# Optimization experiments

Measured on AMD Instinct MI355X. Metric: run time of the kernel, lower is better.

Reference implementation:

```python
import jax, jax.numpy as jnp
import numpy as np

DIM = 128; PDIM = 32; WS = 16; HEADS = 4; NBLK = 2

def gelu(x):
    return jax.nn.gelu(x, approximate=False)  # torch default GELU (erf)

def conv2d(x, w, b=None, pad=0, groups=1):
    y = jax.lax.conv_general_dilated(x, w, (1, 1), [(pad, pad), (pad, pad)],
                                     feature_group_count=groups,
                                     dimension_numbers=('NCHW', 'OIHW', 'NCHW'))
    if b is not None:
        y = y + b[None, :, None, None]
    return y

def layernorm_cf(x, w, b, eps=1e-6):
    # channels_first LayerNorm over C per (b,h,w)
    m = x.mean(axis=1, keepdims=True)
    v = ((x - m) ** 2).mean(axis=1, keepdims=True)
    return (x - m) / jnp.sqrt(v + eps) * w[None, :, None, None] + b[None, :, None, None]

def conv_ffn(x, w1, b1, dw, dwb, w2, b2):
    y = gelu(conv2d(x, w1, b1, 0))
    y = gelu(conv2d(y, dw, dwb, 1, groups=y.shape[1])) + y
    return conv2d(y, w2, b2, 0)

def conv_attention(x, lk, pw1, pb1, pw2, pb2):
    # ConvolutionalAttention (training branch math, non-inplace)
    B, C, H, W = x.shape
    x1, x2 = x[:, :PDIM], x[:, PDIM:]
    # dwc_proj: global avg pool -> 1x1 -> GELU -> 1x1 (pure matmuls on pooled vec)
    v = x1.mean(axis=(2, 3))                              # [B, PDIM]
    h = gelu(v @ pw1[:, :, 0, 0].T + pb1)                 # [B, PDIM//2]
    dk = (h @ pw2[:, :, 0, 0].T + pb2).reshape(B * PDIM, 1, 3, 3)
    # per-sample dynamic depthwise conv via groups = B*PDIM
    dyn = conv2d(x1.reshape(1, B * PDIM, H, W), dk, None, 1,
                 groups=B * PDIM).reshape(B, PDIM, H, W)
    x1 = conv2d(x1, lk, None, lk.shape[-1] // 2) + dyn
    return jnp.concatenate([x1, x2], axis=1)

def window_attention(x, qkv_w, qkv_b, out_w, out_b, table):
    B, C, H, W = x.shape  # H,W divisible by WS -> pad_to_win is a no-op
    hd, wd = H // WS, W // WS
    c = C // HEADS
    qkv = conv2d(x, qkv_w, qkv_b, 0)                      # [B, 3C, H, W]
    qkv = qkv.reshape(B, 3, HEADS, c, hd, WS, wd, WS)
    qkv = qkv.transpose(1, 0, 4, 6, 2, 5, 7, 3).reshape(3, B * hd * wd, HEADS, WS * WS, c)
    q, k, v = qkv[0], qkv[1], qkv[2]
    S = WS * WS
    idx = jnp.arange(S); qh = idx // WS; qw = idx % WS
    rel = (qh[None, :] - qh[:, None] + WS - 1) * (2 * WS - 1) + (qw[None, :] - qw[:, None] + WS - 1)
    bias = table[:, rel]                                  # [HEADS, S, S]
    scores = jnp.einsum('nhqc,nhkc->nhqk', q, k) * (c ** -0.5) + bias[None]
    attn = jax.nn.softmax(scores, axis=-1)
    o = jnp.einsum('nhqk,nhkc->nhqc', attn, v)
    o = o.reshape(B, hd, wd, HEADS, WS, WS, c).transpose(0, 3, 6, 1, 4, 2, 5).reshape(B, C, H, W)
    return conv2d(o, out_w, out_b, 0)

def forward(x, plk_filter, ln_proj_w, ln_proj_b, proj_w1, proj_b1, proj_dw, proj_dwb,
            proj_w2, proj_b2, ln_attn_w, ln_attn_b, qkv_w, qkv_b, attn_out_w, attn_out_b,
            rpe_table, ffn_w1, ffn_b1, ffn_dw, ffn_dwb, ffn_w2, ffn_b2,
            pk_w1, pk_b1, pk_w2, pk_b2, pk_aggr_w, pk_aggr_b,
            ln_out_w, ln_out_b, co_w, co_b):
    skip = x
    x = layernorm_cf(x, ln_proj_w, ln_proj_b)
    x = conv_ffn(x, proj_w1, proj_b1, proj_dw, proj_dwb, proj_w2, proj_b2)
    x = x + window_attention(layernorm_cf(x, ln_attn_w, ln_attn_b),
                             qkv_w, qkv_b, attn_out_w, attn_out_b, rpe_table)
    for i in range(NBLK):
        y = conv_ffn(x, ffn_w1[i], ffn_b1[i], ffn_dw[i], ffn_dwb[i], ffn_w2[i], ffn_b2[i])
        y = conv_attention(y, plk_filter, pk_w1[i], pk_b1[i], pk_w2[i], pk_b2[i])
        y = conv2d(y, pk_aggr_w[i], pk_aggr_b[i], 0)
        x = x + y
    x = conv2d(layernorm_cf(x, ln_out_w, ln_out_b), co_w, co_b, 1)
    return x + skip

def setup_inputs() -> dict:
    key = jax.random.key(0)
    ks = iter(jax.random.split(key, 64))
    def rn(shape, s=0.02):
        return jax.random.normal(next(ks), shape, jnp.float32) * s
    d = DIM; e = 2 * d
    return dict(
        x=jax.random.normal(next(ks), (4, d, 192, 192), jnp.float32),
        plk_filter=rn((PDIM, PDIM, 13, 13), 0.05),
        ln_proj_w=jnp.ones((d,), jnp.float32), ln_proj_b=jnp.zeros((d,), jnp.float32),
        proj_w1=rn((e, d, 1, 1)), proj_b1=rn((e,)),
        proj_dw=rn((e, 1, 3, 3), 0.1), proj_dwb=rn((e,)),
        proj_w2=rn((d, e, 1, 1)), proj_b2=rn((d,)),
        ln_attn_w=jnp.ones((d,), jnp.float32), ln_attn_b=jnp.zeros((d,), jnp.float32),
        qkv_w=rn((3 * d, d, 1, 1)), qkv_b=rn((3 * d,)),
        attn_out_w=rn((d, d, 1, 1)), attn_out_b=rn((d,)),
        rpe_table=rn((HEADS, (2 * WS - 1) ** 2), 0.001),
        ffn_w1=rn((NBLK, e, d, 1, 1)), ffn_b1=rn((NBLK, e)),
        ffn_dw=rn((NBLK, e, 1, 3, 3), 0.1), ffn_dwb=rn((NBLK, e)),
        ffn_w2=rn((NBLK, d, e, 1, 1)), ffn_b2=rn((NBLK, d)),
        pk_w1=rn((NBLK, PDIM // 2, PDIM, 1, 1)), pk_b1=rn((NBLK, PDIM // 2)),
        pk_w2=rn((NBLK, PDIM * 9, PDIM // 2, 1, 1), 0.01), pk_b2=rn((NBLK, PDIM * 9), 0.01),
        pk_aggr_w=rn((NBLK, d, d, 1, 1)), pk_aggr_b=rn((NBLK, d)),
        ln_out_w=jnp.ones((d,), jnp.float32), ln_out_b=jnp.zeros((d,), jnp.float32),
        co_w=rn((d, d, 3, 3), 0.05), co_b=rn((d,)),
    )

def reference(x, plk_filter, ln_proj_w, ln_proj_b, proj_w1, proj_b1, proj_dw, proj_dwb,
              proj_w2, proj_b2, ln_attn_w, ln_attn_b, qkv_w, qkv_b, attn_out_w, attn_out_b,
              rpe_table, ffn_w1, ffn_b1, ffn_dw, ffn_dwb, ffn_w2, ffn_b2,
              pk_w1, pk_b1, pk_w2, pk_b2, pk_aggr_w, pk_aggr_b,
              ln_out_w, ln_out_b, co_w, co_b):
    return forward(x, plk_filter, ln_proj_w, ln_proj_b, proj_w1, proj_b1, proj_dw, proj_dwb,
                   proj_w2, proj_b2, ln_attn_w, ln_attn_b, qkv_w, qkv_b, attn_out_w, attn_out_b,
                   rpe_table, ffn_w1, ffn_b1, ffn_dw, ffn_dwb, ffn_w2, ffn_b2,
                   pk_w1, pk_b1, pk_w2, pk_b2, pk_aggr_w, pk_aggr_b,
                   ln_out_w, ln_out_b, co_w, co_b)
```

## Files before the change

kernel.cpp:

```cpp
#include <hip/hip_runtime.h>
#include <cmath>

#define HWD 192
#define PIX (HWD*HWD)
#define BB  4
#define CCH 128

using short8 = __attribute__((ext_vector_type(8))) short;
using f32x4  = __attribute__((ext_vector_type(4))) float;

__device__ __forceinline__ float gelu_f(float x) {
    return 0.5f * x * (1.0f + erff(x * 0.70710678118654752f));
}
__device__ __forceinline__ unsigned short f2bf(float f) {
    unsigned int u = __float_as_uint(f);
    u += 0x7fff + ((u >> 16) & 1);
    return (unsigned short)(u >> 16);
}
__device__ __forceinline__ float bf2f(unsigned short s) {
    return __uint_as_float((unsigned int)s << 16);
}
__device__ __forceinline__ unsigned pack2bf(float a, float b) {
    return (unsigned)f2bf(a) | ((unsigned)f2bf(b) << 16);
}

__global__ __launch_bounds__(256) void ln_kernel(const float* __restrict__ in,
        const float* __restrict__ w, const float* __restrict__ b,
        unsigned short* __restrict__ out)
{
    int t = blockIdx.x * 256 + threadIdx.x;
    int bi = t / PIX;
    int p  = t - bi*PIX;
    const float* base = in + (size_t)bi * CCH * PIX + p;
    float v[CCH];
    float s = 0.f;
    #pragma unroll
    for (int c=0;c<CCH;++c) { v[c] = base[(size_t)c*PIX]; s += v[c]; }
    float m = s * (1.f/128.f);
    float q = 0.f;
    #pragma unroll
    for (int c=0;c<CCH;++c) { float d = v[c]-m; q += d*d; }
    float iv = rsqrtf(q*(1.f/128.f) + 1e-6f);
    unsigned short* ob = out + (size_t)bi * CCH * PIX + p;
    #pragma unroll
    for (int c=0;c<CCH;++c)
        ob[(size_t)c*PIX] = f2bf((v[c]-m)*iv*w[c] + b[c]);
}

__global__ __launch_bounds__(256) void ln_t_kernel(const float* __restrict__ in,
        const float* __restrict__ w, const float* __restrict__ b,
        unsigned short* __restrict__ outT)
{
    int t = blockIdx.x * 256 + threadIdx.x;
    int bi = t / PIX;
    int p  = t - bi*PIX;
    const float* base = in + (size_t)bi * CCH * PIX + p;
    float v[CCH];
    float s = 0.f;
    #pragma unroll
    for (int c=0;c<CCH;++c) { v[c] = base[(size_t)c*PIX]; s += v[c]; }
    float m = s * (1.f/128.f);
    float q = 0.f;
    #pragma unroll
    for (int c=0;c<CCH;++c) { float d = v[c]-m; q += d*d; }
    float iv = rsqrtf(q*(1.f/128.f) + 1e-6f);
    unsigned short* ob = outT + ((size_t)bi * PIX + p) * 128;
    #pragma unroll
    for (int qq=0; qq<16; ++qq) {
        unsigned short e[8];
        #pragma unroll
        for (int j=0;j<8;++j) {
            int c = qq*8 + j;
            e[j] = f2bf((v[c]-m)*iv*w[c] + b[c]);
        }
        *(uint4*)&ob[qq*8] = *(uint4*)e;
    }
}

template<typename TIN, bool DOGELU, bool DORES, bool OBF, bool WRT32>
__global__ __launch_bounds__(256) void conv1x1_mfma_kernel(
    const TIN* __restrict__ in,
    const unsigned short* __restrict__ wq,
    const float* __restrict__ bias,
    const float* __restrict__ res,
    void* __restrict__ outv,
    unsigned short* __restrict__ yt,
    int Cin)
{
    constexpr int CIP = 136;
    __shared__ unsigned short XL[128*CIP];
    const int Cout = gridDim.y * 128;
    const int px0 = blockIdx.x * 128;
    const int co0 = blockIdx.y * 128;
    const size_t bi = blockIdx.z;
    in  += bi * (size_t)Cin * PIX;
    if (DORES) res += bi * (size_t)Cout * PIX;
    if (WRT32) yt += bi * (size_t)PIX * 32;
    float* outf = (float*)outv + bi * (size_t)Cout * PIX;
    unsigned short* outb = (unsigned short*)outv + bi * (size_t)Cout * PIX;
    const int tid = threadIdx.x;
    const int lane = tid & 63, wid = tid >> 6;
    const int wco = (wid >> 1) * 64;
    const int wpx = (wid & 1) * 64;
    const int l15 = lane & 15, l4 = lane >> 4;

    f32x4 acc[4][4];
    #pragma unroll
    for (int i=0;i<4;++i)
        #pragma unroll
        for (int j=0;j<4;++j) acc[i][j] = (f32x4){0.f,0.f,0.f,0.f};

    for (int k0 = 0; k0 < Cin; k0 += 128) {
        __syncthreads();
        #pragma unroll
        for (int it = 0; it < 4; ++it) {
            int idx = tid + it*256;
            int c2  = idx & 63;
            int s   = idx >> 6;
            const TIN* g0 = in + (size_t)(k0 + c2*2    )*PIX + px0 + s*8;
            const TIN* g1 = in + (size_t)(k0 + c2*2 + 1)*PIX + px0 + s*8;
            unsigned short a8[8], b8[8];
            if constexpr (sizeof(TIN) == 2) {
                *(uint4*)a8 = *(const uint4*)g0;
                *(uint4*)b8 = *(const uint4*)g1;
            } else {
                const float4 f0 = *(const float4*)g0;
                const float4 f1 = *(const float4*)(g0+4);
                const float4 f2 = *(const float4*)g1;
                const float4 f3 = *(const float4*)(g1+4);
                a8[0]=f2bf(f0.x); a8[1]=f2bf(f0.y); a8[2]=f2bf(f0.z); a8[3]=f2bf(f0.w);
                a8[4]=f2bf(f1.x); a8[5]=f2bf(f1.y); a8[6]=f2bf(f1.z); a8[7]=f2bf(f1.w);
                b8[0]=f2bf(f2.x); b8[1]=f2bf(f2.y); b8[2]=f2bf(f2.z); b8[3]=f2bf(f2.w);
                b8[4]=f2bf(f3.x); b8[5]=f2bf(f3.y); b8[6]=f2bf(f3.z); b8[7]=f2bf(f3.w);
            }
            #pragma unroll
            for (int j=0;j<8;++j) {
                unsigned pk = (unsigned)a8[j] | ((unsigned)b8[j] << 16);
                *(unsigned*)&XL[(s*8+j)*CIP + c2*2] = pk;
            }
        }
        __syncthreads();
        #pragma unroll
        for (int ks = 0; ks < 4; ++ks) {
            short8 a[4];
            #pragma unroll
            for (int mt=0; mt<4; ++mt) {
                int co = co0 + wco + mt*16 + l15;
                a[mt] = *(const short8*)(wq + (size_t)co*Cin + k0 + ks*32 + l4*8);
            }
            #pragma unroll
            for (int nt=0; nt<4; ++nt) {
                const short8 b = *(const short8*)&XL[(wpx + nt*16 + l15)*CIP + ks*32 + l4*8];
                #pragma unroll
                for (int mt=0; mt<4; ++mt)
                    acc[mt][nt] = __builtin_amdgcn_mfma_f32_16x16x32_bf16(a[mt], b, acc[mt][nt], 0, 0, 0);
            }
        }
    }
    #pragma unroll
    for (int mt=0; mt<4; ++mt) {
        #pragma unroll
        for (int r=0; r<4; ++r) {
            int co = co0 + wco + mt*16 + l4*4 + r;
            float bs = bias[co];
            #pragma unroll
            for (int nt=0; nt<4; ++nt) {
                int px = px0 + wpx + nt*16 + l15;
                float v = acc[mt][nt][r] + bs;
                if (DOGELU) v = gelu_f(v);
                size_t o = (size_t)co*PIX + px;
                if (DORES) v += res[o];
                if (OBF) {
                    unsigned short bv = f2bf(v);
                    outb[o] = bv;
                    if (WRT32 && co < 32) yt[(size_t)px*32 + co] = bv;
                } else outf[o] = v;
            }
        }
    }
}

__global__ __launch_bounds__(256) void conv3x3_mfma_kernel(
    const unsigned short* __restrict__ inT,
    const unsigned short* __restrict__ wq,
    const float* __restrict__ bias, const float* __restrict__ skip,
    float* __restrict__ out)
{
    constexpr int CIP = 72;
    __shared__ unsigned short XL[4*66*CIP];
    const int x0 = blockIdx.x * 64;
    const int y0 = blockIdx.y * 2;
    const int bi = blockIdx.z;
    const int tid = threadIdx.x;
    const int lane = tid & 63, wid = tid >> 6;
    const int wco = (wid >> 1) * 64;
    const int wrow = wid & 1;
    const int l15 = lane & 15, l4 = lane >> 4;
    const unsigned short* inb = inT + (size_t)bi * PIX * 128;

    f32x4 acc[4][4];
    #pragma unroll
    for (int i=0;i<4;++i)
        #pragma unroll
        for (int j=0;j<4;++j) acc[i][j] = (f32x4){0.f,0.f,0.f,0.f};

    for (int ci0 = 0; ci0 < 128; ci0 += 64) {
        __syncthreads();
        #pragma unroll
        for (int it = 0; it < 9; ++it) {
            int idx = tid + it*256;
            if (idx < 2112) {
                int P = idx >> 3;
                int q = idx & 7;
                int row = P / 66;
                int x = P - row*66;
                int gy = y0 - 1 + row, gx = x0 - 1 + x;
                uint4 v = {0u,0u,0u,0u};
                if ((unsigned)gy < (unsigned)HWD && (unsigned)gx < (unsigned)HWD)
                    v = *(const uint4*)&inb[((size_t)gy*HWD + gx)*128 + ci0 + q*8];
                *(uint4*)&XL[P*CIP + q*8] = v;
            }
        }
        __syncthreads();
        #pragma unroll
        for (int dy=0; dy<3; ++dy) {
            #pragma unroll
            for (int dx=0; dx<3; ++dx) {
                const int rl = wrow + dy;
                #pragma unroll
                for (int ks=0; ks<2; ++ks) {
                    short8 a[4];
                    #pragma unroll
                    for (int mt=0; mt<4; ++mt) {
                        int co = wco + mt*16 + l15;
                        a[mt] = *(const short8*)(wq + ((size_t)co*9 + dy*3+dx)*128 + ci0 + ks*32 + l4*8);
                    }
                    #pragma unroll
                    for (int nt=0; nt<4; ++nt) {
                        const int xl = nt*16 + l15 + dx;
                        const short8 b = *(const short8*)&XL[(rl*66 + xl)*CIP + ks*32 + l4*8];
                        #pragma unroll
                        for (int mt=0; mt<4; ++mt)
                            acc[mt][nt] = __builtin_amdgcn_mfma_f32_16x16x32_bf16(a[mt], b, acc[mt][nt], 0, 0, 0);
                    }
                }
            }
        }
    }
    const int gy = y0 + wrow;
    #pragma unroll
    for (int mt=0; mt<4; ++mt) {
        #pragma unroll
        for (int r=0; r<4; ++r) {
            int co = wco + mt*16 + l4*4 + r;
            float bs = bias[co];
            #pragma unroll
            for (int nt=0; nt<4; ++nt) {
                int gx = x0 + nt*16 + l15;
                size_t o = ((size_t)bi*CCH + co)*PIX + (size_t)gy*HWD + gx;
                out[o] = acc[mt][nt][r] + bs + skip[o];
            }
        }
    }
}

__global__ __launch_bounds__(256) void conv13_mfma_kernel(
    const unsigned short* __restrict__ YT,
    const unsigned short* __restrict__ wq,
    const float* __restrict__ dk,
    unsigned short* __restrict__ outL)
{
    __shared__ unsigned short XL[16*76*32];
    const int x0 = blockIdx.x * 64;
    const int y0 = blockIdx.y * 4;
    const int bi = blockIdx.z;
    const int tid = threadIdx.x;
    const int lane = tid & 63, wr = tid >> 6;
    const int l15 = lane & 15, l4 = lane >> 4;
    const unsigned short* inT = YT + (size_t)bi * PIX * 32;

    #pragma unroll 1
    for (int it = 0; it < 19; ++it) {
        int idx = tid + it*256;
        int P = idx >> 2;
        int q = idx & 3;
        int row = P / 76;
        int x   = P - row*76;
        int gy = y0 - 6 + row, gx = x0 - 6 + x;
        uint4 v = {0u,0u,0u,0u};
        if ((unsigned)gy < (unsigned)HWD && (unsigned)gx < (unsigned)HWD)
            v = *(const uint4*)&inT[((size_t)gy*HWD + gx)*32 + q*8];
        *(uint4*)&XL[P*32 + ((q*8) ^ ((P&3)<<3))] = v;
    }
    __syncthreads();

    f32x4 acc[2][4];
    #pragma unroll
    for (int i=0;i<2;++i)
        #pragma unroll
        for (int j=0;j<4;++j) acc[i][j] = (f32x4){0.f,0.f,0.f,0.f};

    #pragma unroll 1
    for (int dy=0; dy<13; ++dy) {
        const unsigned short* wrow = wq + (size_t)dy*13*1024;
        #pragma unroll
        for (int dx=0; dx<13; ++dx) {
            const short8 a0 = *(const short8*)(wrow + dx*1024 + l15*32 + l4*8);
            const short8 a1 = *(const short8*)(wrow + dx*1024 + (16+l15)*32 + l4*8);
            #pragma unroll
            for (int nt=0; nt<4; ++nt) {
                const int P = (wr + dy)*76 + nt*16 + l15 + dx;
                const short8 b = *(const short8*)&XL[P*32 + ((l4*8) ^ ((P&3)<<3))];
                acc[0][nt] = __builtin_amdgcn_mfma_f32_16x16x32_bf16(a0, b, acc[0][nt], 0, 0, 0);
                acc[1][nt] = __builtin_amdgcn_mfma_f32_16x16x32_bf16(a1, b, acc[1][nt], 0, 0, 0);
            }
        }
    }
    const int gy = y0 + wr;
    #pragma unroll
    for (int mt=0; mt<2; ++mt) {
        #pragma unroll
        for (int r=0; r<4; ++r) {
            const int co = mt*16 + l4*4 + r;
            const float* dkk = dk + (bi*32 + co)*9;
            float k0=dkk[0],k1=dkk[1],k2=dkk[2],k3=dkk[3],k4=dkk[4],
                  k5=dkk[5],k6=dkk[6],k7=dkk[7],k8=dkk[8];
            #pragma unroll
            for (int nt=0; nt<4; ++nt) {
                const int px = nt*16 + l15;
                float dsum = 0.f;
                #pragma unroll
                for (int e=0; e<9; ++e) {
                    int ey = e/3, ex = e - ey*3;
                    int P = (wr+5+ey)*76 + px+5+ex;
                    float pv = bf2f(XL[P*32 + (co ^ ((P&3)<<3))]);
                    float kk = (e==0?k0:e==1?k1:e==2?k2:e==3?k3:e==4?k4:e==5?k5:e==6?k6:e==7?k7:k8);
                    dsum += pv * kk;
                }
                float v = acc[mt][nt][r] + dsum;
                outL[((size_t)bi*CCH + co)*PIX + (size_t)gy*HWD + x0 + px] = f2bf(v);
            }
        }
    }
}

__global__ __launch_bounds__(256) void dw3x3_bf_kernel(const unsigned short* __restrict__ in,
    const float* __restrict__ w, const float* __restrict__ b,
    unsigned short* __restrict__ out)
{
    int t = blockIdx.x*256 + threadIdx.x;
    int pc = t / (PIX/4);
    int p4 = (t - pc*(PIX/4)) * 4;
    int c = pc & 255;
    int y = p4 / HWD, x0 = p4 - y*HWD;
    const unsigned short* ib = in + (size_t)pc * PIX;
    float wk[9];
    #pragma unroll
    for (int e=0;e<9;++e) wk[e] = w[c*9+e];
    float bc = b[c];
    float a0=bc,a1=bc,a2=bc,a3=bc;
    #pragma unroll
    for (int ky=0;ky<3;++ky) {
        int yy = y + ky - 1;
        if ((unsigned)yy < (unsigned)HWD) {
            const unsigned short* row = ib + (size_t)yy*HWD;
            float v[6];
            #pragma unroll
            for (int d=0;d<6;++d) {
                int xx = x0 + d - 1;
                v[d] = ((unsigned)xx < (unsigned)HWD) ? bf2f(row[xx]) : 0.f;
            }
            a0 += v[0]*wk[ky*3+0] + v[1]*wk[ky*3+1] + v[2]*wk[ky*3+2];
            a1 += v[1]*wk[ky*3+0] + v[2]*wk[ky*3+1] + v[3]*wk[ky*3+2];
            a2 += v[2]*wk[ky*3+0] + v[3]*wk[ky*3+1] + v[4]*wk[ky*3+2];
            a3 += v[3]*wk[ky*3+0] + v[4]*wk[ky*3+1] + v[5]*wk[ky*3+2];
        }
    }
    const unsigned short* cen = ib + (size_t)y*HWD + x0;
    unsigned short r0 = f2bf(gelu_f(a0) + bf2f(cen[0]));
    unsigned short r1 = f2bf(gelu_f(a1) + bf2f(cen[1]));
    unsigned short r2 = f2bf(gelu_f(a2) + bf2f(cen[2]));
    unsigned short r3 = f2bf(gelu_f(a3) + bf2f(cen[3]));
    uint2 pk;
    pk.x = (unsigned)r0 | ((unsigned)r1 << 16);
    pk.y = (unsigned)r2 | ((unsigned)r3 << 16);
    *(uint2*)(out + (size_t)pc*PIX + p4) = pk;
}

__global__ __launch_bounds__(256) void attn_mfma_kernel(
    const unsigned short* __restrict__ qkv,
    const float* __restrict__ table,
    unsigned short* __restrict__ o)
{
    __shared__ unsigned short KL[256*40];
    __shared__ unsigned short VL[32*264];
    __shared__ unsigned short PL[4*16*264];
    __shared__ float BT[961];
    __shared__ unsigned short OL[64*33];
    const int win = blockIdx.x, head = blockIdx.y;
    const int bi2 = blockIdx.z >> 2, qc = blockIdx.z & 3;
    const int wy = win/12, wx = win - wy*12;
    qkv += (size_t)bi2 * 384 * PIX;
    o   += (size_t)bi2 * CCH * PIX;
    const unsigned short* qb = qkv + (size_t)(head*32) * PIX;
    const unsigned short* kb = qkv + (size_t)(128 + head*32) * PIX;
    const unsigned short* vb = qkv + (size_t)(256 + head*32) * PIX;
    const int tid = threadIdx.x;

    #pragma unroll
    for (int it = 0; it < 4; ++it) {
        int idx = tid + it*256;
        int c = idx >> 5, seg = idx & 31;
        int k0 = seg*8;
        int sp = ((wy<<4) + (k0>>4))*HWD + (wx<<4) + (k0&15);
        *(uint4*)&VL[c*264 + k0] = *(const uint4*)&vb[(size_t)c*PIX + sp];
    }
    for (int i = tid; i < 8192; i += 256) {
        int c = i >> 8, k = i & 255;
        int sp = ((wy<<4) + (k>>4))*HWD + (wx<<4) + (k&15);
        KL[k*40 + c] = kb[(size_t)c*PIX + sp];
    }
    for (int i = tid; i < 961; i += 256) BT[i] = table[head*961 + i];
    __syncthreads();

    const int lane = tid & 63, w = tid >> 6;
    const int l15 = lane & 15, l4 = lane >> 4;
    const int qi = qc*64 + w*16 + l15;
    const int iy = qi >> 4, ix = qi & 15;
    const int spq = ((wy<<4) + iy)*HWD + (wx<<4) + ix;

    short8 qf;
    #pragma unroll
    for (int j=0;j<8;++j) qf[j] = (short)qb[(size_t)(l4*8+j)*PIX + spq];

    f32x4 s[16];
    #pragma unroll
    for (int nt=0; nt<16; ++nt) {
        const short8 a = *(const short8*)&KL[(nt*16 + l15)*40 + l4*8];
        s[nt] = __builtin_amdgcn_mfma_f32_16x16x32_bf16(a, qf, (f32x4){0.f,0.f,0.f,0.f}, 0, 0, 0);
    }

    const float scale = 0.17677669529663687f;
    float m = -1e30f;
    #pragma unroll
    for (int nt=0; nt<16; ++nt) {
        #pragma unroll
        for (int r=0; r<4; ++r) {
            int k = nt*16 + l4*4 + r;
            float bv = BT[((k>>4) - iy + 15)*31 + ((k&15) - ix + 15)];
            float v = s[nt][r]*scale + bv;
            s[nt][r] = v;
            m = fmaxf(m, v);
        }
    }
    m = fmaxf(m, __shfl_xor(m, 16, 64));
    m = fmaxf(m, __shfl_xor(m, 32, 64));
    float l = 0.f;
    #pragma unroll
    for (int nt=0; nt<16; ++nt) {
        #pragma unroll
        for (int r=0; r<4; ++r) {
            float p = __expf(s[nt][r] - m);
            s[nt][r] = p;
            l += p;
        }
    }
    l += __shfl_xor(l, 16, 64);
    l += __shfl_xor(l, 32, 64);

    unsigned short* PLw = &PL[w*16*264];
    #pragma unroll
    for (int nt=0; nt<16; ++nt) {
        *(unsigned*)&PLw[l15*264 + nt*16 + l4*4]     = pack2bf(s[nt][0], s[nt][1]);
        *(unsigned*)&PLw[l15*264 + nt*16 + l4*4 + 2] = pack2bf(s[nt][2], s[nt][3]);
    }

    f32x4 o0 = (f32x4){0.f,0.f,0.f,0.f}, o1 = (f32x4){0.f,0.f,0.f,0.f};
    #pragma unroll
    for (int kt=0; kt<8; ++kt) {
        const short8 pa = *(const short8*)&PLw[l15*264 + kt*32 + l4*8];
        const short8 v0 = *(const short8*)&VL[l15*264 + kt*32 + l4*8];
        const short8 v1 = *(const short8*)&VL[(16+l15)*264 + kt*32 + l4*8];
        o0 = __builtin_amdgcn_mfma_f32_16x16x32_bf16(pa, v0, o0, 0, 0, 0);
        o1 = __builtin_amdgcn_mfma_f32_16x16x32_bf16(pa, v1, o1, 0, 0, 0);
    }

    #pragma unroll
    for (int r=0; r<4; ++r) {
        float lr = __shfl(l, l4*4 + r, 64);
        float inv = 1.f / lr;
        OL[(w*16 + l4*4 + r)*33 + l15]      = f2bf(o0[r]*inv);
        OL[(w*16 + l4*4 + r)*33 + 16 + l15] = f2bf(o1[r]*inv);
    }
    __syncthreads();

    const int d = tid >> 3, seg = tid & 7;
    const int q0l = seg*8;
    const int qi0 = qc*64 + q0l;
    const int sp0 = ((wy<<4) + (qi0>>4))*HWD + (wx<<4) + (qi0 & 15);
    unsigned short tmp[8];
    #pragma unroll
    for (int j=0;j<8;++j) tmp[j] = OL[(q0l+j)*33 + d];
    *(uint4*)&o[(size_t)(head*32 + d)*PIX + sp0] = *(uint4*)tmp;
}

__global__ __launch_bounds__(256) void meanpool_kernel(const unsigned short* __restrict__ in,
    float* __restrict__ v)
{
    int bc = blockIdx.x;
    int bi = bc >> 5, c = bc & 31;
    const unsigned short* base = in + ((size_t)bi*CCH + c) * PIX;
    float s = 0.f;
    for (int i = threadIdx.x; i < PIX/4; i += 256) {
        const uint2 t4 = ((const uint2*)base)[i];
        s += bf2f((unsigned short)(t4.x & 0xffff)) + bf2f((unsigned short)(t4.x >> 16))
           + bf2f((unsigned short)(t4.y & 0xffff)) + bf2f((unsigned short)(t4.y >> 16));
    }
    #pragma unroll
    for (int off=32; off>0; off>>=1) s += __shfl_down(s, off, 64);
    __shared__ float red[4];
    if ((threadIdx.x & 63) == 0) red[threadIdx.x >> 6] = s;
    __syncthreads();
    if (threadIdx.x == 0) v[bc] = (red[0]+red[1]+red[2]+red[3]) * (1.f/PIX);
}

__global__ __launch_bounds__(256) void mlp_kernel(const float* __restrict__ v,
    const float* __restrict__ pw1, const float* __restrict__ pb1,
    const float* __restrict__ pw2, const float* __restrict__ pb2,
    float* __restrict__ dk)
{
    __shared__ float h[64];
    int tid = threadIdx.x;
    if (tid < 64) {
        int bi = tid >> 4, m = tid & 15;
        float s = pb1[m];
        for (int c=0;c<32;++c) s += v[bi*32+c]*pw1[m*32+c];
        h[tid] = gelu_f(s);
    }
    __syncthreads();
    for (int idx = tid; idx < BB*288; idx += 256) {
        int bi = idx / 288, j = idx - bi*288;
        float s = pb2[j];
        for (int m=0;m<16;++m) s += h[bi*16+m]*pw2[j*16+m];
        dk[idx] = s;
    }
}

__global__ __launch_bounds__(256) void wcast_kernel(const float* __restrict__ w,
    unsigned short* __restrict__ wq, int n)
{
    int idx = blockIdx.x*256 + threadIdx.x;
    if (idx < n) wq[idx] = f2bf(w[idx]);
}

__global__ __launch_bounds__(256) void w3cast_kernel(const float* __restrict__ w,
    unsigned short* __restrict__ wq)
{
    int idx = blockIdx.x*256 + threadIdx.x;
    if (idx >= 128*128*9) return;
    int co = idx / (128*9);
    int rem = idx - co*128*9;
    int ci = rem / 9;
    int tap = rem - ci*9;
    wq[((size_t)co*9 + tap)*128 + ci] = f2bf(w[idx]);
}

__global__ __launch_bounds__(256) void w13cast_kernel(const float* __restrict__ w,
    unsigned short* __restrict__ wq)
{
    int idx = blockIdx.x*256 + threadIdx.x;
    if (idx >= 32*32*169) return;
    int co = idx / (32*169);
    int rem = idx - co*32*169;
    int ci = rem / 169;
    int tap = rem - ci*169;
    wq[((size_t)tap*32 + co)*32 + ci] = f2bf(w[idx]);
}

extern "C" void kernel_launch(void* const* d_in, const int* in_sizes, int n_in,
                              void* d_out, int out_size, void* d_ws, size_t ws_size,
                              hipStream_t stream) {
    (void)in_sizes; (void)n_in; (void)out_size;
    const float* x_in      = (const float*)d_in[0];
    const float* plk       = (const float*)d_in[1];
    const float* ln_proj_w = (const float*)d_in[2];
    const float* ln_proj_b = (const float*)d_in[3];
    const float* proj_w1   = (const float*)d_in[4];
    const float* proj_b1   = (const float*)d_in[5];
    const float* proj_dw   = (const float*)d_in[6];
    const float* proj_dwb  = (const float*)d_in[7];
    const float* proj_w2   = (const float*)d_in[8];
    const float* proj_b2   = (const float*)d_in[9];
    const float* ln_attn_w = (const float*)d_in[10];
    const float* ln_attn_b = (const float*)d_in[11];
    const float* qkv_w     = (const float*)d_in[12];
    const float* qkv_b     = (const float*)d_in[13];
    const float* attn_ow   = (const float*)d_in[14];
    const float* attn_ob   = (const float*)d_in[15];
    const float* rpe       = (const float*)d_in[16];
    const float* ffn_w1    = (const float*)d_in[17];
    const float* ffn_b1    = (const float*)d_in[18];
    const float* ffn_dw    = (const float*)d_in[19];
    const float* ffn_dwb   = (const float*)d_in[20];
    const float* ffn_w2    = (const float*)d_in[21];
    const float* ffn_b2    = (const float*)d_in[22];
    const float* pk_w1     = (const float*)d_in[23];
    const float* pk_b1     = (const float*)d_in[24];
    const float* pk_w2     = (const float*)d_in[25];
    const float* pk_b2     = (const float*)d_in[26];
    const float* aggr_w    = (const float*)d_in[27];
    const float* aggr_b    = (const float*)d_in[28];
    const float* ln_out_w  = (const float*)d_in[29];
    const float* ln_out_b  = (const float*)d_in[30];
    const float* co_w      = (const float*)d_in[31];
    const float* co_b      = (const float*)d_in[32];
    float* out = (float*)d_out;

    const size_t N1b = (size_t)CCH * PIX;
    const size_t RBsz = (size_t)BB * N1b;
    const size_t LNYw = RBsz / 2;
    const size_t POOLw = RBsz;
    const size_t YTw  = (size_t)BB*PIX*32/2;
    const size_t need_floats = RBsz + LNYw + POOLw + YTw + 256 + 1152 + 307712 + 64;
    if (ws_size < need_floats * sizeof(float)) return;

    float* ws  = (float*)d_ws;
    float* RB  = ws;
    unsigned short* LNY  = (unsigned short*)(RB + RBsz);
    unsigned short* POOL = (unsigned short*)(RB + RBsz + LNYw);
    unsigned short* YT   = (unsigned short*)(RB + RBsz + LNYw + POOLw);
    float* VB  = (float*)(RB + RBsz + LNYw + POOLw + YTw);
    float* DK  = VB + 256;
    unsigned short* Q0  = (unsigned short*)(DK + 1152);
    unsigned short* qPW1 = Q0;
    unsigned short* qPW2 = qPW1 + 32768;
    unsigned short* qQKV = qPW2 + 32768;
    unsigned short* qAT  = qQKV + 49152;
    unsigned short* qF1  = qAT  + 16384;
    unsigned short* qF2  = qF1  + 65536;
    unsigned short* qAG  = qF2  + 65536;
    unsigned short* qW3  = qAG  + 32768;
    unsigned short* qW13 = qW3  + 147456;

    unsigned short* E1 = POOL;
    unsigned short* E2 = POOL + (size_t)2*256*PIX;
    unsigned short* QKV = POOL;
    unsigned short* XT  = POOL;

    dim3 blk(256);

    wcast_kernel<<<128, blk, 0, stream>>>(proj_w1, qPW1, 32768);
    wcast_kernel<<<128, blk, 0, stream>>>(proj_w2, qPW2, 32768);
    wcast_kernel<<<192, blk, 0, stream>>>(qkv_w, qQKV, 49152);
    wcast_kernel<<<64,  blk, 0, stream>>>(attn_ow, qAT, 16384);
    wcast_kernel<<<256, blk, 0, stream>>>(ffn_w1, qF1, 65536);
    wcast_kernel<<<256, blk, 0, stream>>>(ffn_w2, qF2, 65536);
    wcast_kernel<<<128, blk, 0, stream>>>(aggr_w, qAG, 32768);
    w3cast_kernel<<<576, blk, 0, stream>>>(co_w, qW3);
    w13cast_kernel<<<676, blk, 0, stream>>>(plk, qW13);

    ln_kernel<<<576, blk, 0, stream>>>(x_in, ln_proj_w, ln_proj_b, LNY);
    for (int h=0; h<2; ++h) {
        conv1x1_mfma_kernel<unsigned short,true,false,true,false><<<dim3(288,2,2), blk, 0, stream>>>(
            LNY + (size_t)h*2*N1b, qPW1, proj_b1, nullptr, E1, nullptr, 128);
        dw3x3_bf_kernel<<<18432, blk, 0, stream>>>(E1, proj_dw, proj_dwb, E2);
        conv1x1_mfma_kernel<unsigned short,false,false,false,false><<<dim3(288,1,2), blk, 0, stream>>>(
            E2, qPW2, proj_b2, nullptr, RB + (size_t)h*2*N1b, nullptr, 256);
    }

    ln_kernel<<<576, blk, 0, stream>>>(RB, ln_attn_w, ln_attn_b, LNY);
    for (int h=0; h<2; ++h) {
        conv1x1_mfma_kernel<unsigned short,false,false,true,false><<<dim3(288,3,2), blk, 0, stream>>>(
            LNY + (size_t)h*2*N1b, qQKV, qkv_b, nullptr, QKV, nullptr, 128);
        attn_mfma_kernel<<<dim3(144,4,8), blk, 0, stream>>>(QKV, rpe, LNY + (size_t)h*2*N1b);
    }
    conv1x1_mfma_kernel<unsigned short,false,true,false,false><<<dim3(288,1,BB), blk, 0, stream>>>(
        LNY, qAT, attn_ob, RB, RB, nullptr, 128);

    for (int i=0;i<2;++i) {
        const float* fb1 = ffn_b1 + (size_t)i*256;
        const float* fdw = ffn_dw + (size_t)i*256*9;
        const float* fdb = ffn_dwb + (size_t)i*256;
        const float* fb2 = ffn_b2 + (size_t)i*128;
        const float* w1i = pk_w1 + (size_t)i*16*32;
        const float* b1i = pk_b1 + (size_t)i*16;
        const float* w2i = pk_w2 + (size_t)i*288*16;
        const float* b2i = pk_b2 + (size_t)i*288;
        const float* abi = aggr_b + (size_t)i*128;

        for (int h=0; h<2; ++h) {
            conv1x1_mfma_kernel<float,true,false,true,false><<<dim3(288,2,2), blk, 0, stream>>>(
                RB + (size_t)h*2*N1b, qF1 + (size_t)i*32768, fb1, nullptr, E1, nullptr, 128);
            dw3x3_bf_kernel<<<18432, blk, 0, stream>>>(E1, fdw, fdb, E2);
            conv1x1_mfma_kernel<unsigned short,false,false,true,true><<<dim3(288,1,2), blk, 0, stream>>>(
                E2, qF2 + (size_t)i*32768, fb2, nullptr, LNY + (size_t)h*2*N1b,
                YT + (size_t)h*2*PIX*32, 256);
        }
        meanpool_kernel<<<BB*32, blk, 0, stream>>>(LNY, VB);
        mlp_kernel<<<1, blk, 0, stream>>>(VB, w1i, b1i, w2i, b2i, DK);
        conv13_mfma_kernel<<<dim3(3,48,BB), blk, 0, stream>>>(YT, qW13, DK, LNY);
        conv1x1_mfma_kernel<unsigned short,false,true,false,false><<<dim3(288,1,BB), blk, 0, stream>>>(
            LNY, qAG + (size_t)i*16384, abi, RB, RB, nullptr, 128);
    }

    ln_t_kernel<<<576, blk, 0, stream>>>(RB, ln_out_w, ln_out_b, XT);
    conv3x3_mfma_kernel<<<dim3(3,96,BB), blk, 0, stream>>>(XT, qW3, co_b, x_in, out);
}
```

Baseline: 1.651 ms.

## Use pixel-major LayerNorm output for 1x1 convs and move the 32-channel transpose out

The proj and qkv LayerNorm stages now write a pixel-major (channel-contiguous) bf16 layout. A new TRANSIN path in the 1x1 MFMA conv loads that layout into LDS with straight 16-byte copies instead of interleaving two channel rows. The conv's K tile drops from 128 to 64, which halves LDS use and may raise occupancy at the cost of more barrier rounds. The scattered per-element 32-channel transposed writes in the FFN second conv are removed and replaced by a separate t32 transpose kernel, which adds one more launch and an extra read of that data.

```diff
diff --git a/kernel.cpp b/kernel.cpp
--- a/kernel.cpp
+++ b/kernel.cpp
@@ -24,9 +24,9 @@
     return (unsigned)f2bf(a) | ((unsigned)f2bf(b) << 16);
 }
 
-__global__ __launch_bounds__(256) void ln_kernel(const float* __restrict__ in,
+__global__ __launch_bounds__(256) void ln_t_kernel(const float* __restrict__ in,
         const float* __restrict__ w, const float* __restrict__ b,
-        unsigned short* __restrict__ out)
+        unsigned short* __restrict__ outT)
 {
     int t = blockIdx.x * 256 + threadIdx.x;
     int bi = t / PIX;
@@ -41,53 +41,44 @@
     #pragma unroll
     for (int c=0;c<CCH;++c) { float d = v[c]-m; q += d*d; }
     float iv = rsqrtf(q*(1.f/128.f) + 1e-6f);
-    unsigned short* ob = out + (size_t)bi * CCH * PIX + p;
-    #pragma unroll
-    for (int c=0;c<CCH;++c)
-        ob[(size_t)c*PIX] = f2bf((v[c]-m)*iv*w[c] + b[c]);
-}
-
-__global__ __launch_bounds__(256) void ln_t_kernel(const float* __restrict__ in,
-        const float* __restrict__ w, const float* __restrict__ b,
-        unsigned short* __restrict__ outT)
+    unsigned short* ob = outT + ((size_t)bi * PIX + p) * 128;
+    #pragma unroll
+    for (int qq=0; qq<16; ++qq) {
+        unsigned short e[8];
+        #pragma unroll
+        for (int j=0;j<8;++j) {
+            int c = qq*8 + j;
+            e[j] = f2bf((v[c]-m)*iv*w[c] + b[c]);
+        }
+        *(uint4*)&ob[qq*8] = *(uint4*)e;
+    }
+}
+
+__global__ __launch_bounds__(256) void t32_kernel(const unsigned short* __restrict__ in,
+    unsigned short* __restrict__ outT)
 {
     int t = blockIdx.x * 256 + threadIdx.x;
     int bi = t / PIX;
     int p  = t - bi*PIX;
-    const float* base = in + (size_t)bi * CCH * PIX + p;
-    float v[CCH];
-    float s = 0.f;
-    #pragma unroll
-    for (int c=0;c<CCH;++c) { v[c] = base[(size_t)c*PIX]; s += v[c]; }
-    float m = s * (1.f/128.f);
-    float q = 0.f;
-    #pragma unroll
-    for (int c=0;c<CCH;++c) { float d = v[c]-m; q += d*d; }
-    float iv = rsqrtf(q*(1.f/128.f) + 1e-6f);
-    unsigned short* ob = outT + ((size_t)bi * PIX + p) * 128;
-    #pragma unroll
-    for (int qq=0; qq<16; ++qq) {
-        unsigned short e[8];
-        #pragma unroll
-        for (int j=0;j<8;++j) {
-            int c = qq*8 + j;
-            e[j] = f2bf((v[c]-m)*iv*w[c] + b[c]);
-        }
-        *(uint4*)&ob[qq*8] = *(uint4*)e;
-    }
-}
-
-template<typename TIN, bool DOGELU, bool DORES, bool OBF, bool WRT32>
+    const unsigned short* base = in + (size_t)bi * CCH * PIX + p;
+    unsigned short e[32];
+    #pragma unroll
+    for (int c=0;c<32;++c) e[c] = base[(size_t)c*PIX];
+    unsigned short* ob = outT + ((size_t)bi * PIX + p) * 32;
+    #pragma unroll
+    for (int q=0;q<4;++q) *(uint4*)&ob[q*8] = *(uint4*)&e[q*8];
+}
+
+template<typename TIN, bool TRANSIN, bool DOGELU, bool DORES, bool OBF>
 __global__ __launch_bounds__(256) void conv1x1_mfma_kernel(
     const TIN* __restrict__ in,
     const unsigned short* __restrict__ wq,
     const float* __restrict__ bias,
     const float* __restrict__ res,
     void* __restrict__ outv,
-    unsigned short* __restrict__ yt,
     int Cin)
 {
-    constexpr int CIP = 136;
+    constexpr int CIP = 72;
     __shared__ unsigned short XL[128*CIP];
     const int Cout = gridDim.y * 128;
     const int px0 = blockIdx.x * 128;
@@ -95,7 +86,6 @@
     const size_t bi = blockIdx.z;
     in  += bi * (size_t)Cin * PIX;
     if (DORES) res += bi * (size_t)Cout * PIX;
-    if (WRT32) yt += bi * (size_t)PIX * 32;
     float* outf = (float*)outv + bi * (size_t)Cout * PIX;
     unsigned short* outb = (unsigned short*)outv + bi * (size_t)Cout * PIX;
     const int tid = threadIdx.x;
@@ -110,38 +100,49 @@
         #pragma unroll
         for (int j=0;j<4;++j) acc[i][j] = (f32x4){0.f,0.f,0.f,0.f};
 
-    for (int k0 = 0; k0 < Cin; k0 += 128) {
+    for (int k0 = 0; k0 < Cin; k0 += 64) {
         __syncthreads();
-        #pragma unroll
-        for (int it = 0; it < 4; ++it) {
-            int idx = tid + it*256;
-            int c2  = idx & 63;
-            int s   = idx >> 6;
-            const TIN* g0 = in + (size_t)(k0 + c2*2    )*PIX + px0 + s*8;
-            const TIN* g1 = in + (size_t)(k0 + c2*2 + 1)*PIX + px0 + s*8;
-            unsigned short a8[8], b8[8];
-            if constexpr (sizeof(TIN) == 2) {
-                *(uint4*)a8 = *(const uint4*)g0;
-                *(uint4*)b8 = *(const uint4*)g1;
-            } else {
-                const float4 f0 = *(const float4*)g0;
-                const float4 f1 = *(const float4*)(g0+4);
-                const float4 f2 = *(const float4*)g1;
-                const float4 f3 = *(const float4*)(g1+4);
-                a8[0]=f2bf(f0.x); a8[1]=f2bf(f0.y); a8[2]=f2bf(f0.z); a8[3]=f2bf(f0.w);
-                a8[4]=f2bf(f1.x); a8[5]=f2bf(f1.y); a8[6]=f2bf(f1.z); a8[7]=f2bf(f1.w);
-                b8[0]=f2bf(f2.x); b8[1]=f2bf(f2.y); b8[2]=f2bf(f2.z); b8[3]=f2bf(f2.w);
-                b8[4]=f2bf(f3.x); b8[5]=f2bf(f3.y); b8[6]=f2bf(f3.z); b8[7]=f2bf(f3.w);
-            }
-            #pragma unroll
-            for (int j=0;j<8;++j) {
-                unsigned pk = (unsigned)a8[j] | ((unsigned)b8[j] << 16);
-                *(unsigned*)&XL[(s*8+j)*CIP + c2*2] = pk;
+        if constexpr (TRANSIN) {
+            #pragma unroll
+            for (int it = 0; it < 4; ++it) {
+                int idx = tid + it*256;
+                int q = idx & 7, px = idx >> 3;
+                const uint4 v = *(const uint4*)((const unsigned short*)in
+                                + ((size_t)(px0 + px))*128 + k0 + q*8);
+                *(uint4*)&XL[px*CIP + q*8] = v;
+            }
+        } else {
+            #pragma unroll
+            for (int it = 0; it < 2; ++it) {
+                int idx = tid + it*256;
+                int c2  = idx & 31;
+                int s   = idx >> 5;
+                const TIN* g0 = in + (size_t)(k0 + c2*2    )*PIX + px0 + s*8;
+                const TIN* g1 = in + (size_t)(k0 + c2*2 + 1)*PIX + px0 + s*8;
+                unsigned short a8[8], b8[8];
+                if constexpr (sizeof(TIN) == 2) {
+                    *(uint4*)a8 = *(const uint4*)g0;
+                    *(uint4*)b8 = *(const uint4*)g1;
+                } else {
+                    const float4 f0 = *(const float4*)g0;
+                    const float4 f1 = *(const float4*)(g0+4);
+                    const float4 f2 = *(const float4*)g1;
+                    const float4 f3 = *(const float4*)(g1+4);
+                    a8[0]=f2bf(f0.x); a8[1]=f2bf(f0.y); a8[2]=f2bf(f0.z); a8[3]=f2bf(f0.w);
+                    a8[4]=f2bf(f1.x); a8[5]=f2bf(f1.y); a8[6]=f2bf(f1.z); a8[7]=f2bf(f1.w);
+                    b8[0]=f2bf(f2.x); b8[1]=f2bf(f2.y); b8[2]=f2bf(f2.z); b8[3]=f2bf(f2.w);
+                    b8[4]=f2bf(f3.x); b8[5]=f2bf(f3.y); b8[6]=f2bf(f3.z); b8[7]=f2bf(f3.w);
+                }
+                #pragma unroll
+                for (int j=0;j<8;++j) {
+                    unsigned pk = (unsigned)a8[j] | ((unsigned)b8[j] << 16);
+                    *(unsigned*)&XL[(s*8+j)*CIP + c2*2] = pk;
+                }
             }
         }
         __syncthreads();
         #pragma unroll
-        for (int ks = 0; ks < 4; ++ks) {
+        for (int ks = 0; ks < 2; ++ks) {
             short8 a[4];
             #pragma unroll
             for (int mt=0; mt<4; ++mt) {
@@ -170,11 +171,8 @@
                 if (DOGELU) v = gelu_f(v);
                 size_t o = (size_t)co*PIX + px;
                 if (DORES) v += res[o];
-                if (OBF) {
-                    unsigned short bv = f2bf(v);
-                    outb[o] = bv;
-                    if (WRT32 && co < 32) yt[(size_t)px*32 + co] = bv;
-                } else outf[o] = v;
+                if (OBF) outb[o] = f2bf(v);
+                else     outf[o] = v;
             }
         }
     }
@@ -659,23 +657,23 @@
     w3cast_kernel<<<576, blk, 0, stream>>>(co_w, qW3);
     w13cast_kernel<<<676, blk, 0, stream>>>(plk, qW13);
 
-    ln_kernel<<<576, blk, 0, stream>>>(x_in, ln_proj_w, ln_proj_b, LNY);
+    ln_t_kernel<<<576, blk, 0, stream>>>(x_in, ln_proj_w, ln_proj_b, LNY);
     for (int h=0; h<2; ++h) {
-        conv1x1_mfma_kernel<unsigned short,true,false,true,false><<<dim3(288,2,2), blk, 0, stream>>>(
-            LNY + (size_t)h*2*N1b, qPW1, proj_b1, nullptr, E1, nullptr, 128);
+        conv1x1_mfma_kernel<unsigned short,true,true,false,true><<<dim3(288,2,2), blk, 0, stream>>>(
+            LNY + (size_t)h*2*N1b, qPW1, proj_b1, nullptr, E1, 128);
         dw3x3_bf_kernel<<<18432, blk, 0, stream>>>(E1, proj_dw, proj_dwb, E2);
         conv1x1_mfma_kernel<unsigned short,false,false,false,false><<<dim3(288,1,2), blk, 0, stream>>>(
-            E2, qPW2, proj_b2, nullptr, RB + (size_t)h*2*N1b, nullptr, 256);
-    }
-
-    ln_kernel<<<576, blk, 0, stream>>>(RB, ln_attn_w, ln_attn_b, LNY);
+            E2, qPW2, proj_b2, nullptr, RB + (size_t)h*2*N1b, 256);
+    }
+
+    ln_t_kernel<<<576, blk, 0, stream>>>(RB, ln_attn_w, ln_attn_b, LNY);
     for (int h=0; h<2; ++h) {
-        conv1x1_mfma_kernel<unsigned short,false,false,true,false><<<dim3(288,3,2), blk, 0, stream>>>(
-            LNY + (size_t)h*2*N1b, qQKV, qkv_b, nullptr, QKV, nullptr, 128);
+        conv1x1_mfma_kernel<unsigned short,true,false,false,true><<<dim3(288,3,2), blk, 0, stream>>>(
+            LNY + (size_t)h*2*N1b, qQKV, qkv_b, nullptr, QKV, 128);
         attn_mfma_kernel<<<dim3(144,4,8), blk, 0, stream>>>(QKV, rpe, LNY + (size_t)h*2*N1b);
     }
-    conv1x1_mfma_kernel<unsigned short,false,true,false,false><<<dim3(288,1,BB), blk, 0, stream>>>(
-        LNY, qAT, attn_ob, RB, RB, nullptr, 128);
+    conv1x1_mfma_kernel<unsigned short,false,false,true,false><<<dim3(288,1,BB), blk, 0, stream>>>(
+        LNY, qAT, attn_ob, RB, RB, 128);
 
     for (int i=0;i<2;++i) {
         const float* fb1 = ffn_b1 + (size_t)i*256;
@@ -689,18 +687,18 @@
         const float* abi = aggr_b + (size_t)i*128;
 
         for (int h=0; h<2; ++h) {
-            conv1x1_mfma_kernel<float,true,false,true,false><<<dim3(288,2,2), blk, 0, stream>>>(
-                RB + (size_t)h*2*N1b, qF1 + (size_t)i*32768, fb1, nullptr, E1, nullptr, 128);
+            conv1x1_mfma_kernel<float,false,true,false,true><<<dim3(288,2,2), blk, 0, stream>>>(
+                RB + (size_t)h*2*N1b, qF1 + (size_t)i*32768, fb1, nullptr, E1, 128);
             dw3x3_bf_kernel<<<18432, blk, 0, stream>>>(E1, fdw, fdb, E2);
-            conv1x1_mfma_kernel<unsigned short,false,false,true,true><<<dim3(288,1,2), blk, 0, stream>>>(
-                E2, qF2 + (size_t)i*32768, fb2, nullptr, LNY + (size_t)h*2*N1b,
-                YT + (size_t)h*2*PIX*32, 256);
-        }
+            conv1x1_mfma_kernel<unsigned short,false,false,false,true><<<dim3(288,1,2), blk, 0, stream>>>(
+                E2, qF2 + (size_t)i*32768, fb2, nullptr, LNY + (size_t)h*2*N1b, 256);
+        }
+        t32_kernel<<<576, blk, 0, stream>>>(LNY, YT);
         meanpool_kernel<<<BB*32, blk, 0, stream>>>(LNY, VB);
         mlp_kernel<<<1, blk, 0, stream>>>(VB, w1i, b1i, w2i, b2i, DK);
         conv13_mfma_kernel<<<dim3(3,48,BB), blk, 0, stream>>>(YT, qW13, DK, LNY);
-        conv1x1_mfma_kernel<unsigned short,false,true,false,false><<<dim3(288,1,BB), blk, 0, stream>>>(
-            LNY, qAG + (size_t)i*16384, abi, RB, RB, nullptr, 128);
+        conv1x1_mfma_kernel<unsigned short,false,false,true,false><<<dim3(288,1,BB), blk, 0, stream>>>(
+            LNY, qAG + (size_t)i*16384, abi, RB, RB, 128);
     }
 
     ln_t_kernel<<<576, blk, 0, stream>>>(RB, ln_out_w, ln_out_b, XT);
```

New measurement: 1.645 ms. About the same (-0.4%).
